# Optimization experiments

Hardware: AMD Instinct MI355X
Metric: run time of the kernel (lower is better)

Reference implementation:

```python
import jax, jax.numpy as jnp
import numpy as np

N_FILTERS = 1024
N_HEADS = 16


def setup_inputs() -> dict:
    key = jax.random.key(0)
    k1, k2, k3 = jax.random.split(key, 3)
    x = jax.random.normal(k1, (8, 1024, N_FILTERS), dtype=jnp.float32)
    # VarianceScaling(0.02) ~ small dense init; 0.02*sqrt(1/fan_in) scale approximated
    w_qkv = jax.random.normal(k2, (N_FILTERS, N_FILTERS * 3), dtype=jnp.float32) * (0.02 / N_FILTERS) ** 0.5
    w_out = jax.random.normal(k3, (N_FILTERS, N_FILTERS), dtype=jnp.float32) * (0.02 / N_FILTERS) ** 0.5
    return {"x": x, "w_qkv": w_qkv, "w_out": w_out}


def reference(x, w_qkv, w_out):
    b, n, c = x.shape
    h = N_HEADS
    d = c // h
    qkv = jnp.einsum('bnc,ce->bne', x, w_qkv)  # [b, n, 3c]
    q, k, v = jnp.split(qkv, 3, axis=-1)
    # b n (h d) -> b h n d
    to_heads = lambda t: t.reshape(b, n, h, d).transpose(0, 2, 1, 3)
    q, k, v = to_heads(q), to_heads(k), to_heads(v)
    scale = jnp.sqrt(jnp.asarray(c, jnp.float32))  # NOTE: sqrt(n_filters), matches source
    attn = jnp.einsum('bhnd,bhmd->bhnm', q, k) / scale
    attn = jax.nn.softmax(attn, axis=-1)
    out = jnp.einsum('bhnm,bhmd->bhnd', attn, v)
    out = out.transpose(0, 2, 1, 3).reshape(b, n, c)  # b h n d -> b n (h d)
    return jnp.einsum('bnc,co->bno', out, w_out)
```

## Files before the change

kernel.cpp:

```cpp
#include <hip/hip_runtime.h>
#include <hip/hip_bf16.h>

typedef __bf16 bf16_t;
typedef __bf16 bf16x8 __attribute__((ext_vector_type(8)));
typedef __bf16 bf16x4 __attribute__((ext_vector_type(4)));
typedef float f32x4 __attribute__((ext_vector_type(4)));

constexpr int LD = 3072;

#define MFMA_16x16x32(a, b, c) __builtin_amdgcn_mfma_f32_16x16x32_bf16((a), (b), (c), 0, 0, 0)

#define GLOAD_LDS16(g, l)                                               \
  __builtin_amdgcn_global_load_lds(                                     \
      (const __attribute__((address_space(1))) void*)(g),               \
      (__attribute__((address_space(3))) void*)(l), 16, 0, 0)

#define TRREAD(dst, addr, imm) \
  asm volatile("ds_read_b64_tr_b16 %0, %1 offset:" imm : "=v"(dst) : "v"(addr))

#define BAR __builtin_amdgcn_s_barrier()
#define LGKM0 do { asm volatile("s_waitcnt lgkmcnt(0)" ::: "memory"); \
                   __builtin_amdgcn_sched_barrier(0); } while (0)

__global__ void cvt_kernel(const float* __restrict__ in, bf16_t* __restrict__ out, int n8) {
  int i = blockIdx.x * blockDim.x + threadIdx.x;
  if (i >= n8) return;
  const float4 a = reinterpret_cast<const float4*>(in)[2 * i];
  const float4 c = reinterpret_cast<const float4*>(in)[2 * i + 1];
  bf16x8 o;
  o[0] = (bf16_t)a.x; o[1] = (bf16_t)a.y; o[2] = (bf16_t)a.z; o[3] = (bf16_t)a.w;
  o[4] = (bf16_t)c.x; o[5] = (bf16_t)c.y; o[6] = (bf16_t)c.z; o[7] = (bf16_t)c.w;
  reinterpret_cast<bf16x8*>(out)[i] = o;
}

__global__ void tcvt_kernel(const float* __restrict__ in, bf16_t* __restrict__ out, int R, int C) {
  __shared__ float tile[32][33];
  const int c0 = blockIdx.x * 32, r0 = blockIdx.y * 32;
  const int tx = threadIdx.x & 31, ty = threadIdx.x >> 5;
#pragma unroll
  for (int i = 0; i < 32; i += 8)
    tile[ty + i][tx] = in[(size_t)(r0 + ty + i) * C + (c0 + tx)];
  __syncthreads();
#pragma unroll
  for (int i = 0; i < 32; i += 8)
    out[(size_t)(c0 + ty + i) * R + (r0 + tx)] = (bf16_t)tile[tx][ty + i];
}

template <typename OutT>
__global__ __launch_bounds__(512, 1) void gemm_bt_128x256(
    const bf16_t* __restrict__ A, const bf16_t* __restrict__ Bt,
    OutT* __restrict__ C, int N, int nrowblk, int q_cols, float q_scale) {
  constexpr int K = 1024;
  extern __shared__ char smem[];
  char* asB = smem;
  char* bsB = smem + 49152;

  const int t = threadIdx.x;
  const int lane = t & 63, wave = t >> 6;
  const int l15 = lane & 15, lg = lane >> 4;
  const int wr = wave >> 2, wc = wave & 3;

  const int cpx = (int)gridDim.x >> 3;
  const int bid = blockIdx.x;
  const int wg = (bid & 7) * cpx + (bid >> 3);
  const int brow = (wg % nrowblk) * 128;
  const int bcol = (wg / nrowblk) * 256;

  const int srow = t >> 3;
  const int schk = (t & 7) ^ (srow & 7);
  const bf16_t* aS = A + (size_t)(brow + srow) * K + schk * 8;
  const bf16_t* bS = Bt + (size_t)(bcol + srow) * K + schk * 8;
  const int ldst = t * 8;

#define STG_A(T, BUF) do {                                               \
    const bf16_t* _s = aS + (T) * 64;                                    \
    bf16_t* _d = (bf16_t*)(asB + (BUF) * 16384) + ldst;                  \
    GLOAD_LDS16(_s, _d);                                                 \
    GLOAD_LDS16(_s + (size_t)64 * K, _d + 4096);                         \
  } while (0)
#define STG_B(T, H, BUF) do {                                            \
    const bf16_t* _s = bS + (size_t)((H) * 128) * K + (T) * 64;          \
    bf16_t* _d = (bf16_t*)(bsB + (BUF) * 32768 + (H) * 16384) + ldst;    \
    GLOAD_LDS16(_s, _d);                                                 \
    GLOAD_LDS16(_s + (size_t)64 * K, _d + 4096);                         \
  } while (0)

  const int rx = l15 & 7;
  const unsigned c0 = ((unsigned)(lg ^ rx)) << 4;
  const unsigned c1 = ((unsigned)((4 | lg) ^ rx)) << 4;
  const unsigned a_rd = (unsigned)(wr * 8192 + l15 * 128);
  const unsigned b_rd = (unsigned)((wc >> 1) * 16384 + (wc & 1) * 8192 + l15 * 128);

  f32x4 acc[4][4] = {};
  bf16x8 af[2][2], bfr[4][2];

#define RD_AF(BUF, MH) do { _Pragma("unroll")                            \
    for (int m = 0; m < 2; ++m) {                                        \
      const char* _p = asB + (BUF) * 16384 + a_rd + ((MH) * 2 + m) * 2048; \
      af[m][0] = *(const bf16x8*)(_p + c0);                              \
      af[m][1] = *(const bf16x8*)(_p + c1); } } while (0)
#define RD_BF(BUF) do { _Pragma("unroll")                                \
    for (int n = 0; n < 4; ++n) {                                        \
      const char* _p = bsB + (BUF) * 32768 + b_rd + n * 2048;            \
      bfr[n][0] = *(const bf16x8*)(_p + c0);                             \
      bfr[n][1] = *(const bf16x8*)(_p + c1); } } while (0)
#define MM(MH) do {                                                      \
    __builtin_amdgcn_s_setprio(1);                                       \
    _Pragma("unroll")                                                    \
    for (int m = 0; m < 2; ++m) { _Pragma("unroll")                      \
      for (int n = 0; n < 4; ++n) {                                      \
        acc[(MH)*2+m][n] =                                               \
            MFMA_16x16x32(af[m][0], bfr[n][0], acc[(MH)*2+m][n]);        \
        acc[(MH)*2+m][n] =                                               \
            MFMA_16x16x32(af[m][1], bfr[n][1], acc[(MH)*2+m][n]); } }    \
    __builtin_amdgcn_s_setprio(0); } while (0)

  STG_A(0, 0); STG_B(0, 0, 0); STG_B(0, 1, 0);
  STG_A(1, 1); STG_B(1, 0, 1); STG_B(1, 1, 1);
  asm volatile("s_waitcnt vmcnt(6)" ::: "memory");
  BAR;

  int bc = 0;
  for (int T = 0; T < 16; ++T) {
    const bool pf = (T + 2 < 16);
    const int bs = (bc >= 1) ? (bc - 1) : 2;
    if (pf) { STG_A(T + 2, bs); STG_B(T + 2, 0, bs); }
    RD_AF(bc, 0);
    RD_BF(bc);
    BAR; LGKM0; MM(0); BAR;
    if (pf) STG_B(T + 2, 1, bs);
    RD_AF(bc, 1);
    BAR; LGKM0; MM(1);
    if (pf) asm volatile("s_waitcnt vmcnt(6)" ::: "memory");
    else    asm volatile("s_waitcnt vmcnt(0)" ::: "memory");
    BAR;
    bc = (bc == 2) ? 0 : bc + 1;
  }

  const float sc = (bcol < q_cols) ? q_scale : 1.0f;
  const int crow0 = brow + wr * 64 + lg * 4;
  const int ccol0 = bcol + wc * 64 + l15;
#pragma unroll
  for (int m = 0; m < 4; ++m)
#pragma unroll
    for (int n = 0; n < 4; ++n)
#pragma unroll
      for (int r = 0; r < 4; ++r)
        C[(size_t)(crow0 + m * 16 + r) * N + ccol0 + n * 16] =
            (OutT)(acc[m][n][r] * sc);
#undef STG_A
#undef STG_B
#undef RD_AF
#undef RD_BF
#undef MM
}

__device__ __forceinline__ unsigned pack_bf16_pair(float a, float b) {
  union { __hip_bfloat162 h; unsigned u; } c;
  c.h = __float22bfloat162_rn(float2{a, b});
  return c.u;
}

__global__ __launch_bounds__(256, 3) void attn_kernel(const bf16_t* __restrict__ qkv,
                                                      bf16_t* __restrict__ ctx) {
  __shared__ bf16_t Ks[2][4096];
  __shared__ bf16_t Vs[2][4096];
  const int tid = threadIdx.x, lane = tid & 63, wave = tid >> 6;
  const int l15 = lane & 15, lg = (lane >> 4) & 3;
  const int flat = blockIdx.x;
  const int xcd = flat & 7, rr = flat >> 3;
  const int qt = rr & 7;
  const int hb = xcd * 16 + (rr >> 3);
  const int h = hb & 15, b = hb >> 4;
  const size_t base = (size_t)b * 1024 * LD;
  const int qbase = qt * 128 + wave * 32;

  bf16x8 qa[2][2];
#pragma unroll
  for (int s = 0; s < 2; s++) {
    const bf16_t* qp = qkv + base + (size_t)(qbase + s * 16 + l15) * LD + h * 64 + lg * 8;
    qa[s][0] = *reinterpret_cast<const bf16x8*>(qp);
    qa[s][1] = *reinterpret_cast<const bf16x8*>(qp + 32);
  }

  const bf16_t* Kb = qkv + base + 1024 + h * 64;
  const bf16_t* Vb = qkv + base + 2048 + h * 64;

  const int krr = lane >> 3;
  const int kcc = (lane & 7) ^ krr;
  const bf16_t* ksrc0 = Kb + (size_t)(wave * 16 + krr) * LD + kcc * 8;
  const bf16_t* ksrc1 = ksrc0 + (size_t)8 * LD;

  const int vd0 = (lane & 1) * 8 + wave * 16;
  const int vkv = ((lane >> 1) & 3) + ((lane >> 3) & 3) * 4 + (lane >> 5) * 16;
  const bf16_t* vsrc0 = Vb + (size_t)vkv * LD + vd0;
  const bf16_t* vsrc1 = vsrc0 + (size_t)32 * LD;

  bf16_t* ksb = &Ks[0][0];
  bf16_t* vsb = &Vs[0][0];
  const char* ksr = (const char*)&Ks[0][0];
  const unsigned vs_byte =
      (unsigned)(size_t)(__attribute__((address_space(3))) void*)(&Vs[0][0]);
  const unsigned tr_lane = vs_byte + lane * 8;

  const int rx7 = l15 & 7;
  const unsigned kb0 = (unsigned)(l15 * 128 + ((lg ^ rx7) << 4));
  const unsigned kb1 = (unsigned)(l15 * 128 + (((4 | lg) ^ rx7) << 4));

  float lr[2] = {0.f, 0.f};
  f32x4 oacc[2][4] = {};

  GLOAD_LDS16(ksrc0, ksb + wave * 1024);
  GLOAD_LDS16(ksrc1, ksb + wave * 1024 + 512);
  GLOAD_LDS16(vsrc0, vsb + wave * 1024);
  GLOAD_LDS16(vsrc1, vsb + wave * 1024 + 512);
  ksrc0 += (size_t)64 * LD; ksrc1 += (size_t)64 * LD;
  vsrc0 += (size_t)64 * LD; vsrc1 += (size_t)64 * LD;
  __syncthreads();

  for (int t = 0; t < 16; t++) {
    const int cur = t & 1;
    if (t < 15) {
      bf16_t* kd = ksb + (cur ^ 1) * 4096 + wave * 1024;
      bf16_t* vd = vsb + (cur ^ 1) * 4096 + wave * 1024;
      GLOAD_LDS16(ksrc0, kd);
      GLOAD_LDS16(ksrc1, kd + 512);
      GLOAD_LDS16(vsrc0, vd);
      GLOAD_LDS16(vsrc1, vd + 512);
      ksrc0 += (size_t)64 * LD; ksrc1 += (size_t)64 * LD;
      vsrc0 += (size_t)64 * LD; vsrc1 += (size_t)64 * LD;
    }

    f32x4 sacc[2][4] = {};
    const char* kt = ksr + cur * 8192;
    __builtin_amdgcn_s_setprio(1);
#pragma unroll
    for (int tt = 0; tt < 4; tt++) {
      const bf16x8 k0 = *reinterpret_cast<const bf16x8*>(kt + tt * 2048 + kb0);
      const bf16x8 k1 = *reinterpret_cast<const bf16x8*>(kt + tt * 2048 + kb1);
      sacc[0][tt] = MFMA_16x16x32(k0, qa[0][0], sacc[0][tt]);
      sacc[0][tt] = MFMA_16x16x32(k1, qa[0][1], sacc[0][tt]);
      sacc[1][tt] = MFMA_16x16x32(k0, qa[1][0], sacc[1][tt]);
      sacc[1][tt] = MFMA_16x16x32(k1, qa[1][1], sacc[1][tt]);
    }
    __builtin_amdgcn_s_setprio(0);

    const unsigned ta = tr_lane + (unsigned)cur * 8192;
    bf16x4 tl0, th0, tl2, th2, tl4, th4, tl6, th6;
    TRREAD(tl0, ta, "0");    TRREAD(th0, ta, "512");
    TRREAD(tl2, ta, "2048"); TRREAD(th2, ta, "2560");
    TRREAD(tl4, ta, "4096"); TRREAD(th4, ta, "4608");
    TRREAD(tl6, ta, "6144"); TRREAD(th6, ta, "6656");
    __builtin_amdgcn_sched_barrier(0);

    unsigned pu[16];
    float ls0 = 0.f, ls1 = 0.f;
#pragma unroll
    for (int tt = 0; tt < 4; tt++) {
      const float a0 = __builtin_exp2f(sacc[0][tt][0]);
      const float a1 = __builtin_exp2f(sacc[0][tt][1]);
      const float a2 = __builtin_exp2f(sacc[0][tt][2]);
      const float a3 = __builtin_exp2f(sacc[0][tt][3]);
      ls0 += (a0 + a1) + (a2 + a3);
      pu[(tt >> 1) * 4 + (tt & 1) * 2 + 0] = pack_bf16_pair(a0, a1);
      pu[(tt >> 1) * 4 + (tt & 1) * 2 + 1] = pack_bf16_pair(a2, a3);
      const float b0 = __builtin_exp2f(sacc[1][tt][0]);
      const float b1 = __builtin_exp2f(sacc[1][tt][1]);
      const float b2 = __builtin_exp2f(sacc[1][tt][2]);
      const float b3 = __builtin_exp2f(sacc[1][tt][3]);
      ls1 += (b0 + b1) + (b2 + b3);
      pu[8 + (tt >> 1) * 4 + (tt & 1) * 2 + 0] = pack_bf16_pair(b0, b1);
      pu[8 + (tt >> 1) * 4 + (tt & 1) * 2 + 1] = pack_bf16_pair(b2, b3);
    }
    lr[0] += ls0;
    lr[1] += ls1;
    bf16x8 pa[2][2];
    pa[0][0] = *reinterpret_cast<bf16x8*>(&pu[0]);
    pa[0][1] = *reinterpret_cast<bf16x8*>(&pu[4]);
    pa[1][0] = *reinterpret_cast<bf16x8*>(&pu[8]);
    pa[1][1] = *reinterpret_cast<bf16x8*>(&pu[12]);

    bf16x4 tl1, th1, tl3, th3, tl5, th5, tl7, th7;
    TRREAD(tl1, ta, "1024"); TRREAD(th1, ta, "1536");
    TRREAD(tl3, ta, "3072"); TRREAD(th3, ta, "3584");
    TRREAD(tl5, ta, "5120"); TRREAD(th5, ta, "5632");
    TRREAD(tl7, ta, "7168"); TRREAD(th7, ta, "7680");

    asm volatile("s_waitcnt lgkmcnt(8)" ::: "memory");
    __builtin_amdgcn_sched_barrier(0);
    {
      bf16x8 vb0[4];
      vb0[0] = __builtin_shufflevector(tl0, th0, 0, 1, 2, 3, 4, 5, 6, 7);
      vb0[1] = __builtin_shufflevector(tl2, th2, 0, 1, 2, 3, 4, 5, 6, 7);
      vb0[2] = __builtin_shufflevector(tl4, th4, 0, 1, 2, 3, 4, 5, 6, 7);
      vb0[3] = __builtin_shufflevector(tl6, th6, 0, 1, 2, 3, 4, 5, 6, 7);
      __builtin_amdgcn_s_setprio(1);
#pragma unroll
      for (int s = 0; s < 2; s++)
#pragma unroll
        for (int dt = 0; dt < 4; dt++)
          oacc[s][dt] = MFMA_16x16x32(pa[s][0], vb0[dt], oacc[s][dt]);
      __builtin_amdgcn_s_setprio(0);
    }

    asm volatile("s_waitcnt lgkmcnt(0)" ::: "memory");
    __builtin_amdgcn_sched_barrier(0);
    {
      bf16x8 vb1[4];
      vb1[0] = __builtin_shufflevector(tl1, th1, 0, 1, 2, 3, 4, 5, 6, 7);
      vb1[1] = __builtin_shufflevector(tl3, th3, 0, 1, 2, 3, 4, 5, 6, 7);
      vb1[2] = __builtin_shufflevector(tl5, th5, 0, 1, 2, 3, 4, 5, 6, 7);
      vb1[3] = __builtin_shufflevector(tl7, th7, 0, 1, 2, 3, 4, 5, 6, 7);
      __builtin_amdgcn_s_setprio(1);
#pragma unroll
      for (int s = 0; s < 2; s++)
#pragma unroll
        for (int dt = 0; dt < 4; dt++)
          oacc[s][dt] = MFMA_16x16x32(pa[s][1], vb1[dt], oacc[s][dt]);
      __builtin_amdgcn_s_setprio(0);
    }

    __syncthreads();
  }

#pragma unroll
  for (int s = 0; s < 2; s++) {
    float v = lr[s];
    v += __shfl_xor(v, 16);
    v += __shfl_xor(v, 32);
#pragma unroll
    for (int r = 0; r < 4; r++) {
      const float inv = 1.0f / __shfl(v, lg * 4 + r);
      const size_t row = (size_t)(b * 1024 + qbase + s * 16 + lg * 4 + r);
#pragma unroll
      for (int dt = 0; dt < 4; dt++)
        ctx[row * 1024 + h * 64 + dt * 16 + l15] = (bf16_t)(oacc[s][dt][r] * inv);
    }
  }
}

extern "C" void kernel_launch(void* const* d_in, const int* in_sizes, int n_in,
                              void* d_out, int out_size, void* d_ws, size_t ws_size,
                              hipStream_t stream) {
  (void)in_sizes; (void)n_in; (void)out_size; (void)ws_size;
  const float* x = (const float*)d_in[0];
  const float* w_qkv = (const float*)d_in[1];
  const float* w_out = (const float*)d_in[2];
  float* out = (float*)d_out;
  char* ws = (char*)d_ws;

  bf16_t* x_b   = (bf16_t*)(ws);
  bf16_t* qkv_b = (bf16_t*)(ws + (size_t)(16 << 20));
  bf16_t* wqT   = (bf16_t*)(ws + (size_t)(64 << 20));
  bf16_t* woT   = (bf16_t*)(ws + (size_t)(70 << 20));
  bf16_t* ctx_b = (bf16_t*)(ws + (size_t)(72 << 20));

  const float qsc = 0.045084220027780106f;

  cvt_kernel<<<8388608 / 8 / 256, 256, 0, stream>>>(x, x_b, 8388608 / 8);
  tcvt_kernel<<<dim3(3072 / 32, 1024 / 32), 256, 0, stream>>>(w_qkv, wqT, 1024, 3072);
  tcvt_kernel<<<dim3(1024 / 32, 1024 / 32), 256, 0, stream>>>(w_out, woT, 1024, 1024);

  gemm_bt_128x256<bf16_t><<<768, 512, 147456, stream>>>(
      x_b, wqT, qkv_b, 3072, 64, 1024, qsc);
  attn_kernel<<<1024, 256, 0, stream>>>(qkv_b, ctx_b);
  gemm_bt_128x256<float><<<256, 512, 147456, stream>>>(
      ctx_b, woT, out, 1024, 64, 0, 1.0f);
}
```

Measured before the change: 168.0 us.

## Use 256x256 QKV GEMM tile and compute softmax denominator via MFMA

Replaces the 128x256 QKV projection GEMM with a dedicated 256x256-tile kernel that uses a finer-grained interleaving of global-to-LDS staging, LDS fragment reads and MFMA quarters within each double-buffered k-step. The aim is more data reuse per loaded tile and better overlap of memory with compute. Separately, the attention kernel now computes the softmax row sums with MFMAs against a vector of ones instead of scalar adds plus cross-lane shuffles. This removes VALU work and shuffles but sums the bf16-rounded probabilities rather than the fp32 ones. The larger tile uses 384 blocks, which may hurt load balance, and adds register pressure from 128 accumulator registers per lane.

```diff
diff --git a/kernel.cpp b/kernel.cpp
--- a/kernel.cpp
+++ b/kernel.cpp
@@ -44,6 +44,129 @@
 #pragma unroll
   for (int i = 0; i < 32; i += 8)
     out[(size_t)(c0 + ty + i) * R + (r0 + tx)] = (bf16_t)tile[tx][ty + i];
+}
+
+__global__ __launch_bounds__(512, 2) void gemm_qkv_256(
+    const bf16_t* __restrict__ A, const bf16_t* __restrict__ Bt,
+    bf16_t* __restrict__ C, float q_scale) {
+  constexpr int K = 1024;
+  extern __shared__ char smem[];
+  char* asB = smem;
+  char* bsB = smem + 65536;
+
+  const int t = threadIdx.x;
+  const int lane = t & 63, wave = t >> 6;
+  const int l15 = lane & 15, lg = lane >> 4;
+  const int wr = wave >> 2, wc = wave & 3;
+
+  const int bid = blockIdx.x;
+  const int wg = (bid & 7) * 48 + (bid >> 3);
+  const int brow = (wg & 31) * 256;
+  const int bcol = (wg >> 5) * 256;
+
+  const int srow = t >> 3;
+  const int schk = (t & 7) ^ (srow & 7);
+  const bf16_t* aS = A + (size_t)(brow + srow) * K + schk * 8;
+  const bf16_t* bS = Bt + (size_t)(bcol + srow) * K + schk * 8;
+  const int ldst = t * 8;
+
+#define STG_A(T, H) do {                                                      \
+    const bf16_t* _s = aS + (size_t)((H) * 128) * K + (T) * 64;               \
+    bf16_t* _d = (bf16_t*)(asB + ((T) & 1) * 32768 + (H) * 16384) + ldst;     \
+    GLOAD_LDS16(_s, _d);                                                      \
+    GLOAD_LDS16(_s + (size_t)64 * K, _d + 4096);                              \
+  } while (0)
+#define STG_B(T, H) do {                                                      \
+    const bf16_t* _s = bS + (size_t)((H) * 128) * K + (T) * 64;               \
+    bf16_t* _d = (bf16_t*)(bsB + ((T) & 1) * 32768 + (H) * 16384) + ldst;     \
+    GLOAD_LDS16(_s, _d);                                                      \
+    GLOAD_LDS16(_s + (size_t)64 * K, _d + 4096);                              \
+  } while (0)
+
+  const int rx = l15 & 7;
+  const unsigned c0 = ((unsigned)(lg ^ rx)) << 4;
+  const unsigned c1 = ((unsigned)((4 | lg) ^ rx)) << 4;
+  const unsigned a_rd = (unsigned)(wr * 16384 + l15 * 128);
+  const unsigned b_rd = (unsigned)((wc >> 1) * 16384 + (wc & 1) * 8192 + l15 * 128);
+
+  f32x4 acc[8][4] = {};
+  bf16x8 af[4][2], bfr[2][2];
+
+#define RD_AF(BUF, MH) do { _Pragma("unroll")                                 \
+    for (int m = 0; m < 4; ++m) {                                             \
+      const char* _p = asB + (BUF) * 32768 + a_rd + ((MH) * 4 + m) * 2048;    \
+      af[m][0] = *(const bf16x8*)(_p + c0);                                   \
+      af[m][1] = *(const bf16x8*)(_p + c1); } } while (0)
+#define RD_BF(BUF, NH) do { _Pragma("unroll")                                 \
+    for (int n = 0; n < 2; ++n) {                                             \
+      const char* _p = bsB + (BUF) * 32768 + b_rd + ((NH) * 2 + n) * 2048;    \
+      bfr[n][0] = *(const bf16x8*)(_p + c0);                                  \
+      bfr[n][1] = *(const bf16x8*)(_p + c1); } } while (0)
+#define MM16(MH, NH) do {                                                     \
+    __builtin_amdgcn_s_setprio(1);                                            \
+    _Pragma("unroll")                                                         \
+    for (int m = 0; m < 4; ++m) { _Pragma("unroll")                           \
+      for (int n = 0; n < 2; ++n) {                                           \
+        acc[(MH)*4+m][(NH)*2+n] =                                             \
+            MFMA_16x16x32(af[m][0], bfr[n][0], acc[(MH)*4+m][(NH)*2+n]);      \
+        acc[(MH)*4+m][(NH)*2+n] =                                             \
+            MFMA_16x16x32(af[m][1], bfr[n][1], acc[(MH)*4+m][(NH)*2+n]); } }  \
+    __builtin_amdgcn_s_setprio(0); } while (0)
+
+  STG_A(0, 0); STG_A(0, 1); STG_B(0, 0); STG_B(0, 1); STG_A(1, 0);
+  asm volatile("s_waitcnt vmcnt(2)" ::: "memory");
+  BAR;
+
+  for (int i = 0; i < 8; ++i) {
+    const int T1 = 2 * i + 1, T2 = 2 * i + 2, T3 = 2 * i + 3;
+    const bool pf = (i < 7);
+    STG_A(T1, 1);
+    RD_AF(0, 0); RD_BF(0, 0);
+    BAR; LGKM0; MM16(0, 0); BAR;
+    STG_B(T1, 0);
+    RD_BF(0, 1);
+    BAR; LGKM0; MM16(0, 1); BAR;
+    STG_B(T1, 1);
+    RD_AF(0, 1);
+    BAR; LGKM0; MM16(1, 1); BAR;
+    if (pf) STG_A(T2, 0);
+    RD_BF(0, 0);
+    BAR; LGKM0; MM16(1, 0);
+    if (pf) asm volatile("s_waitcnt vmcnt(2)" ::: "memory");
+    else    asm volatile("s_waitcnt vmcnt(0)" ::: "memory");
+    BAR;
+    if (pf) STG_A(T2, 1);
+    RD_AF(1, 0); RD_BF(1, 0);
+    BAR; LGKM0; MM16(0, 0); BAR;
+    if (pf) STG_B(T2, 0);
+    RD_BF(1, 1);
+    BAR; LGKM0; MM16(0, 1); BAR;
+    if (pf) STG_B(T2, 1);
+    RD_AF(1, 1);
+    BAR; LGKM0; MM16(1, 1); BAR;
+    if (pf) STG_A(T3, 0);
+    RD_BF(1, 0);
+    BAR; LGKM0; MM16(1, 0);
+    asm volatile("s_waitcnt vmcnt(2)" ::: "memory");
+    BAR;
+  }
+
+  const float sc = (bcol < 1024) ? q_scale : 1.0f;
+  const int crow0 = brow + wr * 128 + lg * 4;
+  const int ccol0 = bcol + wc * 64 + l15;
+#pragma unroll
+  for (int m = 0; m < 8; ++m)
+#pragma unroll
+    for (int n = 0; n < 4; ++n)
+#pragma unroll
+      for (int r = 0; r < 4; ++r)
+        C[(size_t)(crow0 + m * 16 + r) * 3072 + ccol0 + n * 16] =
+            (bf16_t)(acc[m][n][r] * sc);
+#undef STG_A
+#undef STG_B
+#undef RD_AF
+#undef RD_BF
+#undef MM16
 }
 
 template <typename OutT>
@@ -207,7 +330,11 @@
   const unsigned kb0 = (unsigned)(l15 * 128 + ((lg ^ rx7) << 4));
   const unsigned kb1 = (unsigned)(l15 * 128 + (((4 | lg) ^ rx7) << 4));
 
-  float lr[2] = {0.f, 0.f};
+  bf16x8 ones;
+#pragma unroll
+  for (int j = 0; j < 8; j++) ones[j] = (bf16_t)1.0f;
+
+  f32x4 dn[2] = {};
   f32x4 oacc[2][4] = {};
 
   GLOAD_LDS16(ksrc0, ksb + wave * 1024);
@@ -254,31 +381,31 @@
     __builtin_amdgcn_sched_barrier(0);
 
     unsigned pu[16];
-    float ls0 = 0.f, ls1 = 0.f;
 #pragma unroll
     for (int tt = 0; tt < 4; tt++) {
       const float a0 = __builtin_exp2f(sacc[0][tt][0]);
       const float a1 = __builtin_exp2f(sacc[0][tt][1]);
       const float a2 = __builtin_exp2f(sacc[0][tt][2]);
       const float a3 = __builtin_exp2f(sacc[0][tt][3]);
-      ls0 += (a0 + a1) + (a2 + a3);
       pu[(tt >> 1) * 4 + (tt & 1) * 2 + 0] = pack_bf16_pair(a0, a1);
       pu[(tt >> 1) * 4 + (tt & 1) * 2 + 1] = pack_bf16_pair(a2, a3);
       const float b0 = __builtin_exp2f(sacc[1][tt][0]);
       const float b1 = __builtin_exp2f(sacc[1][tt][1]);
       const float b2 = __builtin_exp2f(sacc[1][tt][2]);
       const float b3 = __builtin_exp2f(sacc[1][tt][3]);
-      ls1 += (b0 + b1) + (b2 + b3);
       pu[8 + (tt >> 1) * 4 + (tt & 1) * 2 + 0] = pack_bf16_pair(b0, b1);
       pu[8 + (tt >> 1) * 4 + (tt & 1) * 2 + 1] = pack_bf16_pair(b2, b3);
     }
-    lr[0] += ls0;
-    lr[1] += ls1;
     bf16x8 pa[2][2];
     pa[0][0] = *reinterpret_cast<bf16x8*>(&pu[0]);
     pa[0][1] = *reinterpret_cast<bf16x8*>(&pu[4]);
     pa[1][0] = *reinterpret_cast<bf16x8*>(&pu[8]);
     pa[1][1] = *reinterpret_cast<bf16x8*>(&pu[12]);
+
+    dn[0] = MFMA_16x16x32(pa[0][0], ones, dn[0]);
+    dn[0] = MFMA_16x16x32(pa[0][1], ones, dn[0]);
+    dn[1] = MFMA_16x16x32(pa[1][0], ones, dn[1]);
+    dn[1] = MFMA_16x16x32(pa[1][1], ones, dn[1]);
 
     bf16x4 tl1, th1, tl3, th3, tl5, th5, tl7, th7;
     TRREAD(tl1, ta, "1024"); TRREAD(th1, ta, "1536");
@@ -325,12 +452,9 @@
 
 #pragma unroll
   for (int s = 0; s < 2; s++) {
-    float v = lr[s];
-    v += __shfl_xor(v, 16);
-    v += __shfl_xor(v, 32);
 #pragma unroll
     for (int r = 0; r < 4; r++) {
-      const float inv = 1.0f / __shfl(v, lg * 4 + r);
+      const float inv = 1.0f / dn[s][r];
       const size_t row = (size_t)(b * 1024 + qbase + s * 16 + lg * 4 + r);
 #pragma unroll
       for (int dt = 0; dt < 4; dt++)
@@ -361,8 +485,7 @@
   tcvt_kernel<<<dim3(3072 / 32, 1024 / 32), 256, 0, stream>>>(w_qkv, wqT, 1024, 3072);
   tcvt_kernel<<<dim3(1024 / 32, 1024 / 32), 256, 0, stream>>>(w_out, woT, 1024, 1024);
 
-  gemm_bt_128x256<bf16_t><<<768, 512, 147456, stream>>>(
-      x_b, wqT, qkv_b, 3072, 64, 1024, qsc);
+  gemm_qkv_256<<<384, 512, 131072, stream>>>(x_b, wqT, qkv_b, qsc);
   attn_kernel<<<1024, 256, 0, stream>>>(qkv_b, ctx_b);
   gemm_bt_128x256<float><<<256, 512, 147456, stream>>>(
       ctx_b, woT, out, 1024, 64, 0, 1.0f);
```

Result: faster. 161.6 us (-3.8%).
